# Kernel tuning notes

Measured on AMD Instinct MI355X. Metric: run time of the kernel, lower is better.

## Reference

```python
import jax, jax.numpy as jnp
import numpy as np

NTOKEN = 32000
NHID = 256
L = 128   # leaves per tree (power of 2 -> complete binary tree)
B = 512   # batch


def _postorder_perm(n_leaves):
    """Permutation mapping level-major node order -> stack-machine post-order."""
    levels = int(np.log2(n_leaves))
    sizes = [n_leaves >> l for l in range(levels + 1)]
    offsets = np.concatenate([[0], np.cumsum(sizes)])[:-1]
    order = []

    def rec(l, j):
        if l > 0:
            rec(l - 1, 2 * j)
            rec(l - 1, 2 * j + 1)
        order.append(int(offsets[l] + j))

    rec(levels, 0)
    return np.asarray(order, dtype=np.int32)


def _lstm_combine(hL, cL, hR, cR, W, b):
    # Same math as LSTMOp.forward: Linear(2H -> 5H), 5-way chunk, gates.
    g = jnp.concatenate([hL, hR], axis=-1) @ W + b  # [..., 5H]
    i_, f1_, f2_, o_, u_ = jnp.split(g, 5, axis=-1)
    c = (jax.nn.sigmoid(i_) * jnp.tanh(u_)
         + jax.nn.sigmoid(f1_) * cL
         + jax.nn.sigmoid(f2_) * cR)
    h = jax.nn.sigmoid(o_) * jnp.tanh(c)
    return h, c


def setup_inputs() -> dict:
    key = jax.random.key(0)
    k1, k2, k3, k4 = jax.random.split(key, 4)
    leaf_tokens = jax.random.randint(k1, (L, B), 0, NTOKEN)
    emb = 0.02 * jax.random.normal(k2, (NTOKEN, NHID), dtype=jnp.float32)
    emb_aux = 0.02 * jax.random.normal(k3, (NTOKEN, NHID), dtype=jnp.float32)
    W = jax.random.normal(k4, (2 * NHID, 5 * NHID), dtype=jnp.float32) / np.sqrt(2 * NHID)
    b = jnp.zeros((5 * NHID,), dtype=jnp.float32)
    return {"leaf_tokens": leaf_tokens, "emb": emb, "emb_aux": emb_aux, "W": W, "b": b}


def reference(leaf_tokens, emb, emb_aux, W, b):
    n_leaves, batch = leaf_tokens.shape
    leaves = emb[leaf_tokens]          # [L, B, H]
    leaves_aux = emb_aux[leaf_tokens]  # [L, B, H]

    # Level-by-level combine over the complete binary tree (vectorized across
    # pairs and batch); leaves enter the op as (h, c=0) exactly as in torch.
    h = leaves
    c = jnp.zeros_like(h)
    per_level_h = [h]
    while h.shape[0] > 1:
        h, c = _lstm_combine(h[0::2], c[0::2], h[1::2], c[1::2], W, b)
        per_level_h.append(h)

    all_h = jnp.concatenate(per_level_h, axis=0)        # [2L-1, B, H] level-major
    perm = jnp.asarray(_postorder_perm(n_leaves))
    internal_states = all_h[perm]                       # stack-machine post-order
    root = h[0]                                         # [B, H]

    # All trees have identical (full) length -> masks are all True.
    leaves_mask = jnp.ones((n_leaves, batch), dtype=bool)
    internal_mask = jnp.ones((2 * n_leaves - 1, batch), dtype=bool)
    return root, internal_states, internal_mask, leaves, leaves_aux, leaves_mask
```

## Files before the change

### kernel.cpp

```cpp
#include <hip/hip_runtime.h>
#include <hip/hip_bf16.h>
#include <hip/hip_fp16.h>
#include <cstdint>
#include <cstddef>

#define H 256
#define L 128
#define B 512
#define LEVELS 7
#define BH (B * H)

#define OFF_ROOT 0
#define OFF_INT (B * H)
#define OFF_IMASK (OFF_INT + 255 * BH)
#define OFF_LEAVES (OFF_IMASK + 255 * B)
#define OFF_LAUX (OFF_LEAVES + L * BH)
#define OFF_LMASK (OFF_LAUX + L * BH)

typedef unsigned short u16;
typedef __attribute__((ext_vector_type(8))) _Float16 half8;
typedef __attribute__((ext_vector_type(4))) float f32x4;
typedef __attribute__((ext_vector_type(4))) u16 u16x4;
typedef __attribute__((ext_vector_type(16))) float f32x16;

#if __has_builtin(__builtin_amdgcn_exp2f)
#define EXP2(x) __builtin_amdgcn_exp2f(x)
#else
#define EXP2(x) exp2f(x)
#endif
#if __has_builtin(__builtin_amdgcn_rcpf)
#define RCP(x) __builtin_amdgcn_rcpf(x)
#else
#define RCP(x) (1.0f / (x))
#endif

__device__ __forceinline__ float fsigm(float x) {
    return RCP(1.0f + EXP2(-1.442695041f * x));
}
__device__ __forceinline__ float ftanh(float x) {
    return 1.0f - 2.0f * RCP(1.0f + EXP2(2.885390082f * x));
}


__device__ __forceinline__ int postorder_pos(int level, int j) {
    int start = 0;
    for (int k = level; k <= LEVELS; ++k) {
        if ((j >> (k - level)) & 1) start += (2 << k) - 1;
    }
    return start + (2 << level) - 2;
}

__device__ __forceinline__ u16 f2h(float x) {
    _Float16 h = (_Float16)x;
    u16 u;
    __builtin_memcpy(&u, &h, 2);
    return u;
}
__device__ __forceinline__ float h2f(u16 u) {
    _Float16 h;
    __builtin_memcpy(&h, &u, 2);
    return (float)h;
}

__device__ __forceinline__ void gload16(const void* g, const void* l) {
    __builtin_amdgcn_global_load_lds(
        (const __attribute__((address_space(1))) void*)g,
        (__attribute__((address_space(3))) void*)l, 16, 0, 0);
}

__global__ __launch_bounds__(256) void gather_kernel(
    const int* __restrict__ tok, const float* __restrict__ emb,
    const float* __restrict__ emb_aux, float* __restrict__ out,
    u16* __restrict__ spLeaf) {
    int row = blockIdx.x * 4 + (threadIdx.x >> 6);
    int f4i = threadIdx.x & 63;
    int l = row >> 9, b = row & 511;
    int t = tok[row];
    f32x4 e = *(reinterpret_cast<const f32x4*>(emb + (size_t)t * H) + f4i);
    f32x4 ea = *(reinterpret_cast<const f32x4*>(emb_aux + (size_t)t * H) + f4i);
    __builtin_nontemporal_store(
        e, reinterpret_cast<f32x4*>(out + OFF_LEAVES) + (size_t)row * 64 + f4i);
    __builtin_nontemporal_store(
        ea, reinterpret_cast<f32x4*>(out + OFF_LAUX) + (size_t)row * 64 + f4i);
    int pp = postorder_pos(0, l);
    __builtin_nontemporal_store(
        e, reinterpret_cast<f32x4*>(out + OFF_INT + (size_t)pp * BH +
                                    (size_t)b * H) +
               f4i);
    int ko = f4i >> 2;
    int lanep = (b & 31) + 32 * ((f4i >> 1) & 1);
    int elem0 = 4 * (f4i & 1);
    u16x4 hv;
    hv.x = f2h(e.x); hv.y = f2h(e.y); hv.z = f2h(e.z); hv.w = f2h(e.w);
    u16* np = spLeaf + (size_t)l * BH +
              (size_t)(((b >> 5) * 16 + ko) * 512 + lanep * 8 + elem0);
    *reinterpret_cast<u16x4*>(np) = hv;
}

__global__ __launch_bounds__(256) void wpack_kernel(const float* __restrict__ W,
                                                    u16* __restrict__ wp,
                                                    float* __restrict__ out,
                                                    int* __restrict__ flags) {
    int q = blockIdx.x * 256 + threadIdx.x;
    int k = q / 1280, col = q - k * 1280;
    int gate = col >> 8, hc = col & 255;
    int hcb = hc >> 5, cl = hc & 31;
    int kb = k >> 5, klr = k & 31;
    int ks = klr >> 4, oct = (klr >> 3) & 1, elem = klr & 7;
    size_t off = ((size_t)(hcb * 16 + kb) * 10 + gate * 2 + ks) * 512 +
                 (cl + 32 * oct) * 8 + elem;
    wp[off] = f2h(W[q]);
    if (q < 255 * B) __builtin_nontemporal_store(1.0f, out + OFF_IMASK + q);
    if (q < L * B) __builtin_nontemporal_store(1.0f, out + OFF_LMASK + q);
    if (q < 16) flags[q] = 0;
}

__global__ __launch_bounds__(128) void tree_mega(
    const u16* __restrict__ wp, const float* __restrict__ bias,
    float* __restrict__ out, u16* __restrict__ spA, u16* __restrict__ cAll,
    int* __restrict__ flags, int lev_lo, int lev_hi, int fused) {
    __shared__ __align__(16) u16 Wld[4][10 * 512];

    const int tid = threadIdx.x;
    const int lane = tid & 63;
    const int wm = tid >> 6;
    const int l31 = lane & 31;
    const int lh = lane >> 5;

    auto run_unit = [&](int lev, int p, int b0c, int hcb) {
        const int b0 = b0c * 128;
        const int hc0 = hcb * 32;
        const int cb = 256 - (256 >> (lev - 1));
        const int nid = 256 - (256 >> lev) + p;

        const u16* sL = spA + (size_t)(cb + 2 * p) * BH;
        const u16* sR = sL + BH;

        f32x16 acc[2][5];
#pragma unroll
        for (int nf = 0; nf < 5; ++nf) {
            float bv = bias[nf * H + hc0 + l31];
            f32x16 v;
#pragma unroll
            for (int r = 0; r < 16; ++r) v[r] = bv;
            acc[0][nf] = v;
            acc[1][nf] = v;
        }

        half8 Af[4][2][2];

        auto stage = [&](int buf, int kb) {
            const u16* wsrc = wp + ((size_t)(hcb * 16 + kb) * 10) * 512;
#pragma unroll
            for (int i = 0; i < 5; ++i) {
                int t = 5 * wm + i;
                gload16(wsrc + t * 512 + lane * 8, &Wld[buf][t * 512]);
            }
            const u16* pl = (kb < 8) ? sL : sR;
#pragma unroll
            for (int mf = 0; mf < 2; ++mf)
#pragma unroll
                for (int ks = 0; ks < 2; ++ks) {
                    int T = ((b0 >> 5) + 2 * wm + mf) * 16 + (kb & 7) * 2 + ks;
                    Af[buf][mf][ks] = *reinterpret_cast<const half8*>(
                        pl + (size_t)T * 512 + lane * 8);
                }
        };

        stage(0, 0);
        stage(1, 1);
#pragma unroll
        for (int kb = 0; kb < 16; ++kb) {
            const int cur = kb & 3;
            if (kb < 14) {
                stage((kb + 2) & 3, kb + 2);
                asm volatile("s_waitcnt vmcnt(18)" ::: "memory");
            } else if (kb == 14) {
                asm volatile("s_waitcnt vmcnt(9)" ::: "memory");
            } else {
                asm volatile("s_waitcnt vmcnt(0)" ::: "memory");
            }
            __builtin_amdgcn_s_barrier();
            __builtin_amdgcn_sched_barrier(0);
#pragma unroll
            for (int ks = 0; ks < 2; ++ks)
#pragma unroll
                for (int nf = 0; nf < 5; ++nf) {
                    half8 bf = *reinterpret_cast<const half8*>(
                        &Wld[cur][(nf * 2 + ks) * 512 + lane * 8]);
                    acc[0][nf] = __builtin_amdgcn_mfma_f32_32x32x16_f16(
                        Af[cur][0][ks], bf, acc[0][nf], 0, 0, 0);
                    acc[1][nf] = __builtin_amdgcn_mfma_f32_32x32x16_f16(
                        Af[cur][1][ks], bf, acc[1][nf], 0, 0, 0);
                }
        }

        const int pout = postorder_pos(lev, p);
        float* __restrict__ hout = out + OFF_INT + (size_t)pout * BH;
        u16* __restrict__ cob = cAll + (size_t)(nid - 128) * BH;
        const u16* cLf =
            (lev >= 2) ? cAll + (size_t)(cb + 2 * p - 128) * BH : nullptr;
        const u16* cRf = cLf ? cLf + BH : nullptr;
        u16* __restrict__ soH = (lev < 7) ? spA + (size_t)nid * BH : nullptr;
        const int hc = hc0 + l31;
        const int kop = hcb * 2 + (l31 >> 4);
        const int lpp = 32 * ((l31 >> 3) & 1);
        const int elp = l31 & 7;

#pragma unroll
        for (int mf = 0; mf < 2; ++mf) {
            const int g = (b0 >> 5) + 2 * wm + mf;
            const size_t fbase =
                (((size_t)(g * 8 + hcb) * 8) + lh * 4) * 128 + l31 * 4;
#pragma unroll
            for (int q = 0; q < 4; ++q) {
                float cl4[4] = {0.f, 0.f, 0.f, 0.f};
                float cr4[4] = {0.f, 0.f, 0.f, 0.f};
                if (cLf) {
                    u16x4 a = *reinterpret_cast<const u16x4*>(cLf + fbase +
                                                              q * 128);
                    u16x4 bq = *reinterpret_cast<const u16x4*>(cRf + fbase +
                                                               q * 128);
                    cl4[0] = h2f(a.x); cl4[1] = h2f(a.y);
                    cl4[2] = h2f(a.z); cl4[3] = h2f(a.w);
                    cr4[0] = h2f(bq.x); cr4[1] = h2f(bq.y);
                    cr4[2] = h2f(bq.z); cr4[3] = h2f(bq.w);
                }
                u16x4 co4;
#pragma unroll
                for (int e = 0; e < 4; ++e) {
                    const int r = 4 * q + e;
                    float ig = acc[mf][0][r], f1 = acc[mf][1][r];
                    float f2 = acc[mf][2][r], og = acc[mf][3][r];
                    float ug = acc[mf][4][r];
                    float c = fsigm(ig) * ftanh(ug) + fsigm(f1) * cl4[e] +
                              fsigm(f2) * cr4[e];
                    float hval = fsigm(og) * ftanh(c);
                    co4[e] = f2h(c);
                    const int b = b0 + 64 * wm + 32 * mf + 4 * lh + e + 8 * q;
                    __builtin_nontemporal_store(hval, hout + (size_t)b * H + hc);
                    if (soH)
                        soH[(size_t)((b >> 5) * 16 + kop) * 512 +
                            (size_t)((b & 31) + lpp) * 8 + elp] = f2h(hval);
                    if (lev == LEVELS)
                        __builtin_nontemporal_store(
                            hval, out + OFF_ROOT + (size_t)b * H + hc);
                }
                *reinterpret_cast<u16x4*>(cob + fbase + q * 128) = co4;
            }
        }
    };

    const int nblk = gridDim.x;
    for (int lev = lev_lo; lev <= lev_hi; ++lev) {
        const int n = 128 >> lev;
        if (fused && n >= 8) {
            const int x = blockIdx.x & 7;
            const int ib = blockIdx.x >> 3;
            const int bpx = nblk >> 3;
            const int m = n >> 3;
            for (int j = ib; j < 32 * m; j += bpx) {
                int p = x * m + (j >> 5);
                int inner = j & 31;
                run_unit(lev, p, inner >> 3, inner & 7);
            }
        } else {
            const int units = 32 * n;
            for (int j = blockIdx.x; j < units; j += nblk) {
                run_unit(lev, j >> 5, (j >> 3) & 3, j & 7);
            }
        }
        if (lev < lev_hi) {
            __threadfence();
            __syncthreads();
            if (tid == 0) {
                __hip_atomic_fetch_add(&flags[lev], 1, __ATOMIC_RELEASE,
                                       __HIP_MEMORY_SCOPE_AGENT);
                int it = 0;
                while (__hip_atomic_load(&flags[lev], __ATOMIC_ACQUIRE,
                                         __HIP_MEMORY_SCOPE_AGENT) < nblk &&
                       it < (1 << 24)) {
                    __builtin_amdgcn_s_sleep(8);
                    ++it;
                }
            }
            __syncthreads();
        }
    }
}

extern "C" void kernel_launch(void* const* d_in, const int* in_sizes, int n_in,
                              void* d_out, int out_size, void* d_ws,
                              size_t ws_size, hipStream_t stream) {
    const int* tok = (const int*)d_in[0];
    const float* emb = (const float*)d_in[1];
    const float* emb_aux = (const float*)d_in[2];
    const float* W = (const float*)d_in[3];
    const float* bias = (const float*)d_in[4];
    float* out = (float*)d_out;

    u16* wp = (u16*)d_ws;
    u16* spA = wp + (size_t)655360;
    u16* cAll = spA + (size_t)254 * BH;
    int* flags = (int*)(cAll + (size_t)127 * BH);

    hipLaunchKernelGGL(wpack_kernel, dim3(2560), dim3(256), 0, stream, W, wp,
                       out, flags);
    hipLaunchKernelGGL(gather_kernel, dim3(L * B / 4), dim3(256), 0, stream,
                       tok, emb, emb_aux, out, spA);

    int maxb = 0, ncu = 256, dev = 0;
    (void)hipGetDevice(&dev);
    (void)hipDeviceGetAttribute(&ncu, hipDeviceAttributeMultiprocessorCount,
                                dev);
    (void)hipOccupancyMaxActiveBlocksPerMultiprocessor(&maxb, tree_mega, 128,
                                                       0);
    int grid = maxb * ncu;
    if (grid > 2048) grid = 2048;

    if (maxb >= 1 && grid >= 64) {
        hipLaunchKernelGGL(tree_mega, dim3(grid), dim3(128), 0, stream, wp,
                           bias, out, spA, cAll, flags, 1, LEVELS, 1);
    } else {
        for (int level = 1; level <= LEVELS; ++level) {
            int units = 32 * (L >> level);
            hipLaunchKernelGGL(tree_mega, dim3(units), dim3(128), 0, stream,
                               wp, bias, out, spA, cAll, flags, level, level,
                               0);
        }
    }
}
```

Measured before the change: 312.5 us.

## Replace persistent grid-barrier kernel with one launch per tree level

Drops the persistent megakernel, which synchronised between levels with atomic flag spin-waits, and launches a separate per-level kernel with one block per work unit. Kernel boundaries now order the levels, which removes the spin-barrier cost and the grid-stride loop overhead. In exchange it pays launch overhead for seven launches, and the small upper levels run with few blocks.

```diff
diff --git a/kernel.cpp b/kernel.cpp
--- a/kernel.cpp
+++ b/kernel.cpp
@@ -99,8 +99,7 @@
 
 __global__ __launch_bounds__(256) void wpack_kernel(const float* __restrict__ W,
                                                     u16* __restrict__ wp,
-                                                    float* __restrict__ out,
-                                                    int* __restrict__ flags) {
+                                                    float* __restrict__ out) {
     int q = blockIdx.x * 256 + threadIdx.x;
     int k = q / 1280, col = q - k * 1280;
     int gate = col >> 8, hc = col & 255;
@@ -112,13 +111,12 @@
     wp[off] = f2h(W[q]);
     if (q < 255 * B) __builtin_nontemporal_store(1.0f, out + OFF_IMASK + q);
     if (q < L * B) __builtin_nontemporal_store(1.0f, out + OFF_LMASK + q);
-    if (q < 16) flags[q] = 0;
-}
-
-__global__ __launch_bounds__(128) void tree_mega(
+}
+
+__global__ __launch_bounds__(128) void lstm_level(
     const u16* __restrict__ wp, const float* __restrict__ bias,
     float* __restrict__ out, u16* __restrict__ spA, u16* __restrict__ cAll,
-    int* __restrict__ flags, int lev_lo, int lev_hi, int fused) {
+    int lev) {
     __shared__ __align__(16) u16 Wld[4][10 * 512];
 
     const int tid = threadIdx.x;
@@ -127,164 +125,128 @@
     const int l31 = lane & 31;
     const int lh = lane >> 5;
 
-    auto run_unit = [&](int lev, int p, int b0c, int hcb) {
-        const int b0 = b0c * 128;
-        const int hc0 = hcb * 32;
-        const int cb = 256 - (256 >> (lev - 1));
-        const int nid = 256 - (256 >> lev) + p;
-
-        const u16* sL = spA + (size_t)(cb + 2 * p) * BH;
-        const u16* sR = sL + BH;
-
-        f32x16 acc[2][5];
-#pragma unroll
-        for (int nf = 0; nf < 5; ++nf) {
-            float bv = bias[nf * H + hc0 + l31];
-            f32x16 v;
-#pragma unroll
-            for (int r = 0; r < 16; ++r) v[r] = bv;
-            acc[0][nf] = v;
-            acc[1][nf] = v;
+    const int j = blockIdx.x;
+    const int p = j >> 5;
+    const int b0c = (j >> 3) & 3;
+    const int hcb = j & 7;
+
+    const int b0 = b0c * 128;
+    const int hc0 = hcb * 32;
+    const int cb = 256 - (256 >> (lev - 1));
+    const int nid = 256 - (256 >> lev) + p;
+
+    const u16* sL = spA + (size_t)(cb + 2 * p) * BH;
+    const u16* sR = sL + BH;
+
+    f32x16 acc[2][5];
+#pragma unroll
+    for (int nf = 0; nf < 5; ++nf) {
+        float bv = bias[nf * H + hc0 + l31];
+        f32x16 v;
+#pragma unroll
+        for (int r = 0; r < 16; ++r) v[r] = bv;
+        acc[0][nf] = v;
+        acc[1][nf] = v;
+    }
+
+    half8 Af[4][2][2];
+
+    auto stage = [&](int buf, int kb) {
+        const u16* wsrc = wp + ((size_t)(hcb * 16 + kb) * 10) * 512;
+#pragma unroll
+        for (int i = 0; i < 5; ++i) {
+            int t = 5 * wm + i;
+            gload16(wsrc + t * 512 + lane * 8, &Wld[buf][t * 512]);
         }
-
-        half8 Af[4][2][2];
-
-        auto stage = [&](int buf, int kb) {
-            const u16* wsrc = wp + ((size_t)(hcb * 16 + kb) * 10) * 512;
-#pragma unroll
-            for (int i = 0; i < 5; ++i) {
-                int t = 5 * wm + i;
-                gload16(wsrc + t * 512 + lane * 8, &Wld[buf][t * 512]);
-            }
-            const u16* pl = (kb < 8) ? sL : sR;
-#pragma unroll
-            for (int mf = 0; mf < 2; ++mf)
-#pragma unroll
-                for (int ks = 0; ks < 2; ++ks) {
-                    int T = ((b0 >> 5) + 2 * wm + mf) * 16 + (kb & 7) * 2 + ks;
-                    Af[buf][mf][ks] = *reinterpret_cast<const half8*>(
-                        pl + (size_t)T * 512 + lane * 8);
-                }
-        };
-
-        stage(0, 0);
-        stage(1, 1);
-#pragma unroll
-        for (int kb = 0; kb < 16; ++kb) {
-            const int cur = kb & 3;
-            if (kb < 14) {
-                stage((kb + 2) & 3, kb + 2);
-                asm volatile("s_waitcnt vmcnt(18)" ::: "memory");
-            } else if (kb == 14) {
-                asm volatile("s_waitcnt vmcnt(9)" ::: "memory");
-            } else {
-                asm volatile("s_waitcnt vmcnt(0)" ::: "memory");
-            }
-            __builtin_amdgcn_s_barrier();
-            __builtin_amdgcn_sched_barrier(0);
-#pragma unroll
-            for (int ks = 0; ks < 2; ++ks)
-#pragma unroll
-                for (int nf = 0; nf < 5; ++nf) {
-                    half8 bf = *reinterpret_cast<const half8*>(
-                        &Wld[cur][(nf * 2 + ks) * 512 + lane * 8]);
-                    acc[0][nf] = __builtin_amdgcn_mfma_f32_32x32x16_f16(
-                        Af[cur][0][ks], bf, acc[0][nf], 0, 0, 0);
-                    acc[1][nf] = __builtin_amdgcn_mfma_f32_32x32x16_f16(
-                        Af[cur][1][ks], bf, acc[1][nf], 0, 0, 0);
-                }
+        const u16* pl = (kb < 8) ? sL : sR;
+#pragma unroll
+        for (int mf = 0; mf < 2; ++mf)
+#pragma unroll
+            for (int ks = 0; ks < 2; ++ks) {
+                int T = ((b0 >> 5) + 2 * wm + mf) * 16 + (kb & 7) * 2 + ks;
+                Af[buf][mf][ks] = *reinterpret_cast<const half8*>(
+                    pl + (size_t)T * 512 + lane * 8);
+            }
+    };
+
+    stage(0, 0);
+    stage(1, 1);
+#pragma unroll
+    for (int kb = 0; kb < 16; ++kb) {
+        const int cur = kb & 3;
+        if (kb < 14) {
+            stage((kb + 2) & 3, kb + 2);
+            asm volatile("s_waitcnt vmcnt(18)" ::: "memory");
+        } else if (kb == 14) {
+            asm volatile("s_waitcnt vmcnt(9)" ::: "memory");
+        } else {
+            asm volatile("s_waitcnt vmcnt(0)" ::: "memory");
         }
-
-        const int pout = postorder_pos(lev, p);
-        float* __restrict__ hout = out + OFF_INT + (size_t)pout * BH;
-        u16* __restrict__ cob = cAll + (size_t)(nid - 128) * BH;
-        const u16* cLf =
-            (lev >= 2) ? cAll + (size_t)(cb + 2 * p - 128) * BH : nullptr;
-        const u16* cRf = cLf ? cLf + BH : nullptr;
-        u16* __restrict__ soH = (lev < 7) ? spA + (size_t)nid * BH : nullptr;
-        const int hc = hc0 + l31;
-        const int kop = hcb * 2 + (l31 >> 4);
-        const int lpp = 32 * ((l31 >> 3) & 1);
-        const int elp = l31 & 7;
-
-#pragma unroll
-        for (int mf = 0; mf < 2; ++mf) {
-            const int g = (b0 >> 5) + 2 * wm + mf;
-            const size_t fbase =
-                (((size_t)(g * 8 + hcb) * 8) + lh * 4) * 128 + l31 * 4;
-#pragma unroll
-            for (int q = 0; q < 4; ++q) {
-                float cl4[4] = {0.f, 0.f, 0.f, 0.f};
-                float cr4[4] = {0.f, 0.f, 0.f, 0.f};
-                if (cLf) {
-                    u16x4 a = *reinterpret_cast<const u16x4*>(cLf + fbase +
-                                                              q * 128);
-                    u16x4 bq = *reinterpret_cast<const u16x4*>(cRf + fbase +
-                                                               q * 128);
-                    cl4[0] = h2f(a.x); cl4[1] = h2f(a.y);
-                    cl4[2] = h2f(a.z); cl4[3] = h2f(a.w);
-                    cr4[0] = h2f(bq.x); cr4[1] = h2f(bq.y);
-                    cr4[2] = h2f(bq.z); cr4[3] = h2f(bq.w);
-                }
-                u16x4 co4;
-#pragma unroll
-                for (int e = 0; e < 4; ++e) {
-                    const int r = 4 * q + e;
-                    float ig = acc[mf][0][r], f1 = acc[mf][1][r];
-                    float f2 = acc[mf][2][r], og = acc[mf][3][r];
-                    float ug = acc[mf][4][r];
-                    float c = fsigm(ig) * ftanh(ug) + fsigm(f1) * cl4[e] +
-                              fsigm(f2) * cr4[e];
-                    float hval = fsigm(og) * ftanh(c);
-                    co4[e] = f2h(c);
-                    const int b = b0 + 64 * wm + 32 * mf + 4 * lh + e + 8 * q;
-                    __builtin_nontemporal_store(hval, hout + (size_t)b * H + hc);
-                    if (soH)
-                        soH[(size_t)((b >> 5) * 16 + kop) * 512 +
-                            (size_t)((b & 31) + lpp) * 8 + elp] = f2h(hval);
-                    if (lev == LEVELS)
-                        __builtin_nontemporal_store(
-                            hval, out + OFF_ROOT + (size_t)b * H + hc);
-                }
-                *reinterpret_cast<u16x4*>(cob + fbase + q * 128) = co4;
-            }
-        }
-    };
-
-    const int nblk = gridDim.x;
-    for (int lev = lev_lo; lev <= lev_hi; ++lev) {
-        const int n = 128 >> lev;
-        if (fused && n >= 8) {
-            const int x = blockIdx.x & 7;
-            const int ib = blockIdx.x >> 3;
-            const int bpx = nblk >> 3;
-            const int m = n >> 3;
-            for (int j = ib; j < 32 * m; j += bpx) {
-                int p = x * m + (j >> 5);
-                int inner = j & 31;
-                run_unit(lev, p, inner >> 3, inner & 7);
-            }
-        } else {
-            const int units = 32 * n;
-            for (int j = blockIdx.x; j < units; j += nblk) {
-                run_unit(lev, j >> 5, (j >> 3) & 3, j & 7);
-            }
-        }
-        if (lev < lev_hi) {
-            __threadfence();
-            __syncthreads();
-            if (tid == 0) {
-                __hip_atomic_fetch_add(&flags[lev], 1, __ATOMIC_RELEASE,
-                                       __HIP_MEMORY_SCOPE_AGENT);
-                int it = 0;
-                while (__hip_atomic_load(&flags[lev], __ATOMIC_ACQUIRE,
-                                         __HIP_MEMORY_SCOPE_AGENT) < nblk &&
-                       it < (1 << 24)) {
-                    __builtin_amdgcn_s_sleep(8);
-                    ++it;
-                }
-            }
-            __syncthreads();
+        __builtin_amdgcn_s_barrier();
+        __builtin_amdgcn_sched_barrier(0);
+#pragma unroll
+        for (int ks = 0; ks < 2; ++ks)
+#pragma unroll
+            for (int nf = 0; nf < 5; ++nf) {
+                half8 bf = *reinterpret_cast<const half8*>(
+                    &Wld[cur][(nf * 2 + ks) * 512 + lane * 8]);
+                acc[0][nf] = __builtin_amdgcn_mfma_f32_32x32x16_f16(
+                    Af[cur][0][ks], bf, acc[0][nf], 0, 0, 0);
+                acc[1][nf] = __builtin_amdgcn_mfma_f32_32x32x16_f16(
+                    Af[cur][1][ks], bf, acc[1][nf], 0, 0, 0);
+            }
+    }
+
+    const int pout = postorder_pos(lev, p);
+    float* __restrict__ hout = out + OFF_INT + (size_t)pout * BH;
+    u16* __restrict__ cob = cAll + (size_t)(nid - 128) * BH;
+    const u16* cLf =
+        (lev >= 2) ? cAll + (size_t)(cb + 2 * p - 128) * BH : nullptr;
+    const u16* cRf = cLf ? cLf + BH : nullptr;
+    u16* __restrict__ soH = (lev < 7) ? spA + (size_t)nid * BH : nullptr;
+    const int hc = hc0 + l31;
+    const int kop = hcb * 2 + (l31 >> 4);
+    const int lpp = 32 * ((l31 >> 3) & 1);
+    const int elp = l31 & 7;
+
+#pragma unroll
+    for (int mf = 0; mf < 2; ++mf) {
+        const int g = (b0 >> 5) + 2 * wm + mf;
+        const size_t fbase =
+            (((size_t)(g * 8 + hcb) * 8) + lh * 4) * 128 + l31 * 4;
+#pragma unroll
+        for (int q = 0; q < 4; ++q) {
+            float cl4[4] = {0.f, 0.f, 0.f, 0.f};
+            float cr4[4] = {0.f, 0.f, 0.f, 0.f};
+            if (cLf) {
+                u16x4 a = *reinterpret_cast<const u16x4*>(cLf + fbase + q * 128);
+                u16x4 bq = *reinterpret_cast<const u16x4*>(cRf + fbase + q * 128);
+                cl4[0] = h2f(a.x); cl4[1] = h2f(a.y);
+                cl4[2] = h2f(a.z); cl4[3] = h2f(a.w);
+                cr4[0] = h2f(bq.x); cr4[1] = h2f(bq.y);
+                cr4[2] = h2f(bq.z); cr4[3] = h2f(bq.w);
+            }
+            u16x4 co4;
+#pragma unroll
+            for (int e = 0; e < 4; ++e) {
+                const int r = 4 * q + e;
+                float ig = acc[mf][0][r], f1 = acc[mf][1][r];
+                float f2 = acc[mf][2][r], og = acc[mf][3][r];
+                float ug = acc[mf][4][r];
+                float c = fsigm(ig) * ftanh(ug) + fsigm(f1) * cl4[e] +
+                          fsigm(f2) * cr4[e];
+                float hval = fsigm(og) * ftanh(c);
+                co4[e] = f2h(c);
+                const int b = b0 + 64 * wm + 32 * mf + 4 * lh + e + 8 * q;
+                __builtin_nontemporal_store(hval, hout + (size_t)b * H + hc);
+                if (soH)
+                    soH[(size_t)((b >> 5) * 16 + kop) * 512 +
+                        (size_t)((b & 31) + lpp) * 8 + elp] = f2h(hval);
+                if (lev == LEVELS)
+                    __builtin_nontemporal_store(
+                        hval, out + OFF_ROOT + (size_t)b * H + hc);
+            }
+            *reinterpret_cast<u16x4*>(cob + fbase + q * 128) = co4;
         }
     }
 }
@@ -302,31 +264,15 @@
     u16* wp = (u16*)d_ws;
     u16* spA = wp + (size_t)655360;
     u16* cAll = spA + (size_t)254 * BH;
-    int* flags = (int*)(cAll + (size_t)127 * BH);
 
     hipLaunchKernelGGL(wpack_kernel, dim3(2560), dim3(256), 0, stream, W, wp,
-                       out, flags);
+                       out);
     hipLaunchKernelGGL(gather_kernel, dim3(L * B / 4), dim3(256), 0, stream,
                        tok, emb, emb_aux, out, spA);
 
-    int maxb = 0, ncu = 256, dev = 0;
-    (void)hipGetDevice(&dev);
-    (void)hipDeviceGetAttribute(&ncu, hipDeviceAttributeMultiprocessorCount,
-                                dev);
-    (void)hipOccupancyMaxActiveBlocksPerMultiprocessor(&maxb, tree_mega, 128,
-                                                       0);
-    int grid = maxb * ncu;
-    if (grid > 2048) grid = 2048;
-
-    if (maxb >= 1 && grid >= 64) {
-        hipLaunchKernelGGL(tree_mega, dim3(grid), dim3(128), 0, stream, wp,
-                           bias, out, spA, cAll, flags, 1, LEVELS, 1);
-    } else {
-        for (int level = 1; level <= LEVELS; ++level) {
-            int units = 32 * (L >> level);
-            hipLaunchKernelGGL(tree_mega, dim3(units), dim3(128), 0, stream,
-                               wp, bias, out, spA, cAll, flags, level, level,
-                               0);
-        }
-    }
-}
+    for (int level = 1; level <= LEVELS; ++level) {
+        int units = 32 * (L >> level);
+        hipLaunchKernelGGL(lstm_level, dim3(units), dim3(128), 0, stream, wp,
+                           bias, out, spA, cAll, level);
+    }
+}
```

Measured after the change: 277.3 us. 11.3% less time.
